# Performance work log

Hardware: AMD Instinct MI355X
Metric: run time of the kernel (lower is better)

Reference implementation:

```python
import jax, jax.numpy as jnp
import numpy as np

B, T = 256, 512
V, H, L, O = 29275, 128, 2, 3


def setup_inputs() -> dict:
    key = jax.random.key(0)
    ks = jax.random.split(key, 8)
    s_emb = 1.0  # torch nn.Embedding default init is N(0,1)
    s = 1.0 / np.sqrt(H)  # torch GRU/Linear default U(-1/sqrt(H), 1/sqrt(H))
    return {
        "x": jax.random.randint(ks[0], (B, T), 0, V, dtype=jnp.int32),
        "emb": jax.random.normal(ks[1], (V, H), dtype=jnp.float32) * s_emb,
        "W_ih": jax.random.uniform(ks[2], (L, 3 * H, H), jnp.float32, -s, s),
        "W_hh": jax.random.uniform(ks[3], (L, 3 * H, H), jnp.float32, -s, s),
        "b_ih": jax.random.uniform(ks[4], (L, 3 * H), jnp.float32, -s, s),
        "b_hh": jax.random.uniform(ks[5], (L, 3 * H), jnp.float32, -s, s),
        "fc_w": jax.random.uniform(ks[6], (O, H), jnp.float32, -s, s),
        "fc_b": jax.random.uniform(ks[7], (O,), jnp.float32, -s, s),
    }


def _gru_layer(inp, Wih, Whh, bih, bhh):
    # inp: [B, T, H]. PyTorch GRU gate order: r, z, n.
    gx = jnp.einsum("bth,gh->btg", inp, Wih) + bih  # [B, T, 3H] input-side gates

    def step(h, gx_t):
        gh = h @ Whh.T + bhh  # [B, 3H]
        xr, xz, xn = jnp.split(gx_t, 3, axis=-1)
        hr, hz, hn = jnp.split(gh, 3, axis=-1)
        r = jax.nn.sigmoid(xr + hr)
        z = jax.nn.sigmoid(xz + hz)
        n = jnp.tanh(xn + r * hn)
        h_new = (1.0 - z) * n + z * h
        return h_new, h_new

    h0 = jnp.zeros((inp.shape[0], Whh.shape[1]), dtype=inp.dtype)
    _, outs = jax.lax.scan(step, h0, gx.transpose(1, 0, 2))  # [T, B, H]
    return outs.transpose(1, 0, 2)


def reference(x, emb, W_ih, W_hh, b_ih, b_hh, fc_w, fc_b):
    h = emb[x]  # [B, T, H] embedding lookup
    for l in range(L):  # small fixed layer count; dropout inactive in eval mode
        h = _gru_layer(h, W_ih[l], W_hh[l], b_ih[l], b_hh[l])
    last = jax.nn.relu(h[:, -1])  # [B, H]
    return last @ fc_w.T + fc_b  # [B, O]
```

## Files before the change

### kernel.cpp

```cpp
#include <hip/hip_runtime.h>
#include <hip/hip_bf16.h>

#define B_   256
#define T_   512
#define H_   128
#define G3_  384

#define TM   128
#define TN   128
#define TK   32
#define LDA  132

typedef float v4f __attribute__((ext_vector_type(4)));

__device__ __forceinline__ float fast_rcp(float x) {
    return __builtin_amdgcn_rcpf(x);
}
__device__ __forceinline__ float sigmoid_f(float x) {
    return fast_rcp(1.0f + __expf(-x));
}
__device__ __forceinline__ float tanh_f(float x) {
    return fmaf(-2.0f, fast_rcp(__expf(2.0f * x) + 1.0f), 1.0f);
}

__device__ __forceinline__ float bfly_fold4(float v) {
    int x;
    x = __builtin_amdgcn_update_dpp(0, __float_as_int(v), 0x0B1, 0xF, 0xF, true);
    v += __int_as_float(x);
    x = __builtin_amdgcn_update_dpp(0, __float_as_int(v), 0x04E, 0xF, 0xF, true);
    v += __int_as_float(x);
    return v;
}

#define DOT4(acc, hv, wv)                                        \
    acc = fmaf((hv).x, (wv).x, acc);                             \
    acc = fmaf((hv).y, (wv).y, acc);                             \
    acc = fmaf((hv).z, (wv).z, acc);                             \
    acc = fmaf((hv).w, (wv).w, acc);

template<bool GATHER>
__global__ __launch_bounds__(256, 2)
void gx_gemm(const float* __restrict__ X,
             const int*   __restrict__ idx,
             const float* __restrict__ emb,
             const float* __restrict__ W,
             const float* __restrict__ bias,
             float*       __restrict__ gx)
{
    __shared__ __align__(16) float As[2][TK][LDA];
    __shared__ __align__(16) float Bs[2][TK][LDA];

    const int tid = threadIdx.x;
    const int tn  = tid & 15;
    const int tm  = tid >> 4;
    const int n0  = blockIdx.x * TN;
    const int m0  = blockIdx.y * TM;

    const int q  = tid & 7;
    const float* rowA[4];
    const float* rowB[4];
#pragma unroll
    for (int s = 0; s < 4; s++) {
        const int r = (tid >> 3) + 32 * s;
        rowA[s] = GATHER ? (emb + (size_t)idx[m0 + r] * H_)
                         : (X + (size_t)(m0 + r) * H_);
        rowB[s] = W + (size_t)(n0 + r) * H_;
    }

    float4 stA[4], stB[4];
    auto load_chunk = [&](int kc) {
#pragma unroll
        for (int s = 0; s < 4; s++) {
            stA[s] = *(const float4*)(rowA[s] + kc + q * 4);
            stB[s] = *(const float4*)(rowB[s] + kc + q * 4);
        }
    };
    auto store_chunk = [&](int buf) {
#pragma unroll
        for (int s = 0; s < 4; s++) {
            const int r = (tid >> 3) + 32 * s;
#pragma unroll
            for (int d = 0; d < 4; d++) {
                As[buf][q * 4 + d][r] = ((const float*)&stA[s])[d];
                Bs[buf][q * 4 + d][r] = ((const float*)&stB[s])[d];
            }
        }
    };

    float4 acc[2][2][4];
#pragma unroll
    for (int a = 0; a < 2; a++)
#pragma unroll
        for (int b = 0; b < 2; b++)
#pragma unroll
            for (int c = 0; c < 4; c++) acc[a][b][c] = make_float4(0.f, 0.f, 0.f, 0.f);

    load_chunk(0);
    store_chunk(0);
    __syncthreads();

    for (int c = 0; c < 4; c++) {
        if (c < 3) load_chunk((c + 1) * TK);
        const int buf = c & 1;
#pragma unroll 4
        for (int k = 0; k < TK; k++) {
            float4 a0 = *(const float4*)&As[buf][k][tm * 4];
            float4 a1 = *(const float4*)&As[buf][k][64 + tm * 4];
            float4 b0 = *(const float4*)&Bs[buf][k][tn * 4];
            float4 b1 = *(const float4*)&Bs[buf][k][64 + tn * 4];
            float4 av[2] = {a0, a1}, bv[2] = {b0, b1};
#pragma unroll
            for (int mg = 0; mg < 2; mg++)
#pragma unroll
                for (int mi = 0; mi < 4; mi++) {
                    const float am = ((const float*)&av[mg])[mi];
#pragma unroll
                    for (int ng = 0; ng < 2; ng++) {
                        acc[mg][ng][mi].x = fmaf(am, bv[ng].x, acc[mg][ng][mi].x);
                        acc[mg][ng][mi].y = fmaf(am, bv[ng].y, acc[mg][ng][mi].y);
                        acc[mg][ng][mi].z = fmaf(am, bv[ng].z, acc[mg][ng][mi].z);
                        acc[mg][ng][mi].w = fmaf(am, bv[ng].w, acc[mg][ng][mi].w);
                    }
                }
        }
        if (c < 3) {
            store_chunk(buf ^ 1);
            __syncthreads();
        }
    }

    const float4 bb0 = *(const float4*)(bias + n0 + tn * 4);
    const float4 bb1 = *(const float4*)(bias + n0 + 64 + tn * 4);
#pragma unroll
    for (int mg = 0; mg < 2; mg++)
#pragma unroll
        for (int mi = 0; mi < 4; mi++) {
            const int m = m0 + mg * 64 + tm * 4 + mi;
            float* dst = gx + (size_t)m * G3_ + n0;
            float4 v0 = acc[mg][0][mi];
            v0.x += bb0.x; v0.y += bb0.y; v0.z += bb0.z; v0.w += bb0.w;
            float4 v1 = acc[mg][1][mi];
            v1.x += bb1.x; v1.y += bb1.y; v1.z += bb1.z; v1.w += bb1.w;
            *(float4*)(dst + tn * 4) = v0;
            *(float4*)(dst + 64 + tn * 4) = v1;
        }
}

template<bool STORE_H, bool FINAL>
__global__ __launch_bounds__(512)
__attribute__((amdgpu_waves_per_eu(2, 2)))
void gru_rec(const float* __restrict__ gx,
             const float* __restrict__ Whh,
             const float* __restrict__ bhh,
             float*       __restrict__ hseq,
             const float* __restrict__ fc_w,
             const float* __restrict__ fc_b,
             float*       __restrict__ out)
{
    __shared__ __align__(16) float h2[2][H_];

    const int tid = threadIdx.x;
    const int b   = blockIdx.x;
    const int jg  = tid >> 2;
    const int ks  = tid & 3;

    const v4f* wr = (const v4f*)(Whh + (size_t)(jg      ) * H_ + ks * 32);
    const v4f* wz = (const v4f*)(Whh + (size_t)(jg + 128) * H_ + ks * 32);
    const v4f* wn = (const v4f*)(Whh + (size_t)(jg + 256) * H_ + ks * 32);
    v4f Wr[8], Wz[8], Wn[8];
#pragma unroll
    for (int c = 0; c < 8; c++) { Wr[c] = wr[c]; Wz[c] = wz[c]; Wn[c] = wn[c]; }

    const float bhr = bhh[jg];
    const float bhz = bhh[jg + 128];
    const float bhn = bhh[jg + 256];

    const float* gxb = gx + (size_t)b * T_ * G3_;
    float gr = gxb[jg], gz = gxb[jg + 128], gn = gxb[jg + 256];
    float h_old = 0.0f;

    if (tid < H_) h2[0][tid] = 0.0f;

    const int hw = ((jg >> 2) & 7) * 16 + (jg >> 5) * 4 + (jg & 3);
    const int hb = ks * 4;

    const float* gnx = gxb + G3_;
    float* hp = STORE_H ? (hseq + (size_t)b * T_ * H_ + jg) : nullptr;

    __syncthreads();

#define GRU_STEP(HIN, HOUT)                                                   \
    {                                                                         \
        const float gr2_ = gnx[jg];                                           \
        const float gz2_ = gnx[jg + 128];                                     \
        const float gn2_ = gnx[jg + 256];                                     \
        gnx += G3_;                                                           \
        float p0 = 0.f, p1 = 0.f, p2 = 0.f;                                   \
        _Pragma("unroll")                                                     \
        for (int c = 0; c < 8; c++) {                                         \
            float4 hv = *(const float4*)&(HIN)[16 * c + hb];                  \
            DOT4(p0, hv, Wr[c]) DOT4(p1, hv, Wz[c]) DOT4(p2, hv, Wn[c])      \
        }                                                                     \
        p0 = bfly_fold4(p0);                                                  \
        p1 = bfly_fold4(p1);                                                  \
        p2 = bfly_fold4(p2);                                                  \
        const float r_ = sigmoid_f(gr + p0 + bhr);                            \
        const float z_ = sigmoid_f(gz + p1 + bhz);                            \
        const float n_ = tanh_f(gn + r_ * (p2 + bhn));                        \
        h_old = (1.0f - z_) * n_ + z_ * h_old;                                \
        if (ks == 0) {                                                        \
            (HOUT)[hw] = h_old;                                               \
            if (STORE_H) *hp = h_old;                                         \
        }                                                                     \
        if (STORE_H) hp += H_;                                                \
        gr = gr2_; gz = gz2_; gn = gn2_;                                      \
        __syncthreads();                                                      \
    }

    for (int t = 0; t < T_; t += 2) {
        asm volatile("" : "+v"(Wr[0]), "+v"(Wr[1]), "+v"(Wr[2]), "+v"(Wr[3]),
                          "+v"(Wr[4]), "+v"(Wr[5]), "+v"(Wr[6]), "+v"(Wr[7]),
                          "+v"(Wz[0]), "+v"(Wz[1]), "+v"(Wz[2]), "+v"(Wz[3]),
                          "+v"(Wz[4]), "+v"(Wz[5]), "+v"(Wz[6]), "+v"(Wz[7]),
                          "+v"(Wn[0]), "+v"(Wn[1]), "+v"(Wn[2]), "+v"(Wn[3]),
                          "+v"(Wn[4]), "+v"(Wn[5]), "+v"(Wn[6]), "+v"(Wn[7]));
        GRU_STEP(h2[0], h2[1])
        GRU_STEP(h2[1], h2[0])
    }
#undef GRU_STEP

    if (FINAL) {
        if (ks == 0) h2[1][jg] = fmaxf(h_old, 0.0f);
        __syncthreads();
        if (tid < 3) {
            float acc = fc_b[tid];
            const float* fw = fc_w + tid * H_;
#pragma unroll
            for (int k = 0; k < H_; k++) acc = fmaf(h2[1][k], fw[k], acc);
            out[b * 3 + tid] = acc;
        }
    }
}

extern "C" void kernel_launch(void* const* d_in, const int* in_sizes, int n_in,
                              void* d_out, int out_size, void* d_ws, size_t ws_size,
                              hipStream_t stream)
{
    const int*   x    = (const int*)  d_in[0];
    const float* emb  = (const float*)d_in[1];
    const float* W_ih = (const float*)d_in[2];
    const float* W_hh = (const float*)d_in[3];
    const float* b_ih = (const float*)d_in[4];
    const float* b_hh = (const float*)d_in[5];
    const float* fc_w = (const float*)d_in[6];
    const float* fc_b = (const float*)d_in[7];
    float* out = (float*)d_out;

    const int M = B_ * T_;
    const size_t gx_f32 = (size_t)M * G3_ * sizeof(float);

    float* gx = (float*)d_ws;
    float* h1 = (float*)((char*)d_ws + gx_f32);

    dim3 ggx(G3_ / TN, M / TM);
    dim3 bgx(256);
    dim3 grec(B_), brec(512);

    hipLaunchKernelGGL((gx_gemm<true>), ggx, bgx, 0, stream,
                       nullptr, x, emb, W_ih, b_ih, gx);
    hipLaunchKernelGGL((gru_rec<true, false>), grec, brec, 0, stream,
                       gx, W_hh, b_hh, h1, nullptr, nullptr, nullptr);
    hipLaunchKernelGGL((gx_gemm<false>), ggx, bgx, 0, stream,
                       h1, nullptr, nullptr, W_ih + G3_ * H_, b_ih + G3_, gx);
    hipLaunchKernelGGL((gru_rec<false, true>), grec, brec, 0, stream,
                       gx, W_hh + G3_ * H_, b_hh + G3_, nullptr, fc_w, fc_b, out);
}
```

Before: 935.8 us.

## Split recurrent GEMV 8-way over K with two hidden units per thread group

After: 999.4 us. 6.8% more time.

```diff
diff --git a/kernel.cpp b/kernel.cpp
--- a/kernel.cpp
+++ b/kernel.cpp
@@ -23,11 +23,13 @@
     return fmaf(-2.0f, fast_rcp(__expf(2.0f * x) + 1.0f), 1.0f);
 }
 
-__device__ __forceinline__ float bfly_fold4(float v) {
+__device__ __forceinline__ float bfly_fold8(float v) {
     int x;
     x = __builtin_amdgcn_update_dpp(0, __float_as_int(v), 0x0B1, 0xF, 0xF, true);
     v += __int_as_float(x);
     x = __builtin_amdgcn_update_dpp(0, __float_as_int(v), 0x04E, 0xF, 0xF, true);
+    v += __int_as_float(x);
+    x = __builtin_amdgcn_update_dpp(0, __float_as_int(v), 0x141, 0xF, 0xF, true);
     v += __int_as_float(x);
     return v;
 }
@@ -161,56 +163,94 @@
 
     const int tid = threadIdx.x;
     const int b   = blockIdx.x;
-    const int jg  = tid >> 2;
-    const int ks  = tid & 3;
-
-    const v4f* wr = (const v4f*)(Whh + (size_t)(jg      ) * H_ + ks * 32);
-    const v4f* wz = (const v4f*)(Whh + (size_t)(jg + 128) * H_ + ks * 32);
-    const v4f* wn = (const v4f*)(Whh + (size_t)(jg + 256) * H_ + ks * 32);
-    v4f Wr[8], Wz[8], Wn[8];
-#pragma unroll
-    for (int c = 0; c < 8; c++) { Wr[c] = wr[c]; Wz[c] = wz[c]; Wn[c] = wn[c]; }
-
-    const float bhr = bhh[jg];
-    const float bhz = bhh[jg + 128];
-    const float bhn = bhh[jg + 256];
+    const int jg2 = tid >> 3;
+    const int ks  = tid & 7;
+    const int j0  = jg2 * 2;
+    const int rot = ks >> 1;
+
+    v4f W0r[4], W0z[4], W0n[4], W1r[4], W1z[4], W1n[4];
+    {
+        const float* r0 = Whh + (size_t)(j0      ) * H_ + ks * 16;
+        const float* z0 = Whh + (size_t)(j0 + 128) * H_ + ks * 16;
+        const float* n0 = Whh + (size_t)(j0 + 256) * H_ + ks * 16;
+#pragma unroll
+        for (int c = 0; c < 4; c++) {
+            const int f = ((c + rot) & 3) * 4;
+            W0r[c] = *(const v4f*)(r0 + f);
+            W0z[c] = *(const v4f*)(z0 + f);
+            W0n[c] = *(const v4f*)(n0 + f);
+            W1r[c] = *(const v4f*)(r0 + H_ + f);
+            W1z[c] = *(const v4f*)(z0 + H_ + f);
+            W1n[c] = *(const v4f*)(n0 + H_ + f);
+        }
+    }
+
+    const float2 bhr = *(const float2*)(bhh + j0);
+    const float2 bhz = *(const float2*)(bhh + j0 + H_);
+    const float2 bhn = *(const float2*)(bhh + j0 + 2 * H_);
 
     const float* gxb = gx + (size_t)b * T_ * G3_;
-    float gr = gxb[jg], gz = gxb[jg + 128], gn = gxb[jg + 256];
-    float h_old = 0.0f;
+    const float* gp  = gxb + j0;
+    float2 gr = *(const float2*)(gp);
+    float2 gz = *(const float2*)(gp + H_);
+    float2 gn = *(const float2*)(gp + 2 * H_);
+    gp += G3_;
+    float2 h_old; h_old.x = 0.0f; h_old.y = 0.0f;
 
     if (tid < H_) h2[0][tid] = 0.0f;
 
-    const int hw = ((jg >> 2) & 7) * 16 + (jg >> 5) * 4 + (jg & 3);
-    const int hb = ks * 4;
-
-    const float* gnx = gxb + G3_;
-    float* hp = STORE_H ? (hseq + (size_t)b * T_ * H_ + jg) : nullptr;
+    const int ho0 = ks * 16 + (((0 + rot) & 3) << 2);
+    const int ho1 = ks * 16 + (((1 + rot) & 3) << 2);
+    const int ho2 = ks * 16 + (((2 + rot) & 3) << 2);
+    const int ho3 = ks * 16 + (((3 + rot) & 3) << 2);
+
+    float* hp = STORE_H ? (hseq + (size_t)b * T_ * H_ + j0) : nullptr;
 
     __syncthreads();
+
+    asm volatile("" : "+v"(W0r[0]), "+v"(W0r[1]), "+v"(W0r[2]), "+v"(W0r[3]),
+                      "+v"(W0z[0]), "+v"(W0z[1]), "+v"(W0z[2]), "+v"(W0z[3]),
+                      "+v"(W0n[0]), "+v"(W0n[1]), "+v"(W0n[2]), "+v"(W0n[3]),
+                      "+v"(W1r[0]), "+v"(W1r[1]), "+v"(W1r[2]), "+v"(W1r[3]),
+                      "+v"(W1z[0]), "+v"(W1z[1]), "+v"(W1z[2]), "+v"(W1z[3]),
+                      "+v"(W1n[0]), "+v"(W1n[1]), "+v"(W1n[2]), "+v"(W1n[3]));
 
 #define GRU_STEP(HIN, HOUT)                                                   \
     {                                                                         \
-        const float gr2_ = gnx[jg];                                           \
-        const float gz2_ = gnx[jg + 128];                                     \
-        const float gn2_ = gnx[jg + 256];                                     \
-        gnx += G3_;                                                           \
-        float p0 = 0.f, p1 = 0.f, p2 = 0.f;                                   \
-        _Pragma("unroll")                                                     \
-        for (int c = 0; c < 8; c++) {                                         \
-            float4 hv = *(const float4*)&(HIN)[16 * c + hb];                  \
-            DOT4(p0, hv, Wr[c]) DOT4(p1, hv, Wz[c]) DOT4(p2, hv, Wn[c])      \
+        const float2 gr2_ = *(const float2*)(gp);                             \
+        const float2 gz2_ = *(const float2*)(gp + H_);                        \
+        const float2 gn2_ = *(const float2*)(gp + 2 * H_);                    \
+        gp += G3_;                                                            \
+        float p0r = 0.f, p0z = 0.f, p0n = 0.f;                                \
+        float p1r = 0.f, p1z = 0.f, p1n = 0.f;                                \
+        {                                                                     \
+            float4 hv;                                                        \
+            hv = *(const float4*)&(HIN)[ho0];                                 \
+            DOT4(p0r, hv, W0r[0]) DOT4(p0z, hv, W0z[0]) DOT4(p0n, hv, W0n[0])\
+            DOT4(p1r, hv, W1r[0]) DOT4(p1z, hv, W1z[0]) DOT4(p1n, hv, W1n[0])\
+            hv = *(const float4*)&(HIN)[ho1];                                 \
+            DOT4(p0r, hv, W0r[1]) DOT4(p0z, hv, W0z[1]) DOT4(p0n, hv, W0n[1])\
+            DOT4(p1r, hv, W1r[1]) DOT4(p1z, hv, W1z[1]) DOT4(p1n, hv, W1n[1])\
+            hv = *(const float4*)&(HIN)[ho2];                                 \
+            DOT4(p0r, hv, W0r[2]) DOT4(p0z, hv, W0z[2]) DOT4(p0n, hv, W0n[2])\
+            DOT4(p1r, hv, W1r[2]) DOT4(p1z, hv, W1z[2]) DOT4(p1n, hv, W1n[2])\
+            hv = *(const float4*)&(HIN)[ho3];                                 \
+            DOT4(p0r, hv, W0r[3]) DOT4(p0z, hv, W0z[3]) DOT4(p0n, hv, W0n[3])\
+            DOT4(p1r, hv, W1r[3]) DOT4(p1z, hv, W1z[3]) DOT4(p1n, hv, W1n[3])\
         }                                                                     \
-        p0 = bfly_fold4(p0);                                                  \
-        p1 = bfly_fold4(p1);                                                  \
-        p2 = bfly_fold4(p2);                                                  \
-        const float r_ = sigmoid_f(gr + p0 + bhr);                            \
-        const float z_ = sigmoid_f(gz + p1 + bhz);                            \
-        const float n_ = tanh_f(gn + r_ * (p2 + bhn));                        \
-        h_old = (1.0f - z_) * n_ + z_ * h_old;                                \
+        p0r = bfly_fold8(p0r); p0z = bfly_fold8(p0z); p0n = bfly_fold8(p0n);  \
+        p1r = bfly_fold8(p1r); p1z = bfly_fold8(p1z); p1n = bfly_fold8(p1n);  \
+        const float r0_ = sigmoid_f(gr.x + p0r + bhr.x);                      \
+        const float z0_ = sigmoid_f(gz.x + p0z + bhz.x);                      \
+        const float n0_ = tanh_f(gn.x + r0_ * (p0n + bhn.x));                 \
+        h_old.x = (1.0f - z0_) * n0_ + z0_ * h_old.x;                         \
+        const float r1_ = sigmoid_f(gr.y + p1r + bhr.y);                      \
+        const float z1_ = sigmoid_f(gz.y + p1z + bhz.y);                      \
+        const float n1_ = tanh_f(gn.y + r1_ * (p1n + bhn.y));                 \
+        h_old.y = (1.0f - z1_) * n1_ + z1_ * h_old.y;                         \
         if (ks == 0) {                                                        \
-            (HOUT)[hw] = h_old;                                               \
-            if (STORE_H) *hp = h_old;                                         \
+            *(float2*)&(HOUT)[j0] = h_old;                                    \
+            if (STORE_H) *(float2*)hp = h_old;                                \
         }                                                                     \
         if (STORE_H) hp += H_;                                                \
         gr = gr2_; gz = gz2_; gn = gn2_;                                      \
@@ -218,19 +258,16 @@
     }
 
     for (int t = 0; t < T_; t += 2) {
-        asm volatile("" : "+v"(Wr[0]), "+v"(Wr[1]), "+v"(Wr[2]), "+v"(Wr[3]),
-                          "+v"(Wr[4]), "+v"(Wr[5]), "+v"(Wr[6]), "+v"(Wr[7]),
-                          "+v"(Wz[0]), "+v"(Wz[1]), "+v"(Wz[2]), "+v"(Wz[3]),
-                          "+v"(Wz[4]), "+v"(Wz[5]), "+v"(Wz[6]), "+v"(Wz[7]),
-                          "+v"(Wn[0]), "+v"(Wn[1]), "+v"(Wn[2]), "+v"(Wn[3]),
-                          "+v"(Wn[4]), "+v"(Wn[5]), "+v"(Wn[6]), "+v"(Wn[7]));
         GRU_STEP(h2[0], h2[1])
         GRU_STEP(h2[1], h2[0])
     }
 #undef GRU_STEP
 
     if (FINAL) {
-        if (ks == 0) h2[1][jg] = fmaxf(h_old, 0.0f);
+        if (ks == 0) {
+            h2[1][j0]     = fmaxf(h_old.x, 0.0f);
+            h2[1][j0 + 1] = fmaxf(h_old.y, 0.0f);
+        }
         __syncthreads();
         if (tid < 3) {
             float acc = fc_b[tid];
```
